# Kernel optimization log

Measured on AMD Instinct MI355X. Metric: run time of the kernel, lower is better.

## Reference

```python
import jax, jax.numpy as jnp
import numpy as np

B, L, D, H = 32, 1024, 1024, 1024

def setup_inputs() -> dict:
    key = jax.random.key(0)
    k1, k2, k3 = jax.random.split(key, 3)
    query = jax.random.normal(k1, (B, L, D), dtype=jnp.float32)
    keys = jax.random.normal(k2, (B, L, D), dtype=jnp.float32)
    # xavier_normal for Linear(D, H): std = sqrt(2/(D+H))
    W = jax.random.normal(k3, (H, D), dtype=jnp.float32) * np.sqrt(2.0 / (D + H)).astype(np.float32)
    b = jnp.zeros((H,), dtype=jnp.float32)
    return {"query": query, "keys": keys, "W": W, "b": b}

def reference(query, keys, W, b):
    # L2-normalize along feature dim (matches torch .norm(dim=-1, keepdim=True))
    qn = query / jnp.linalg.norm(query, axis=-1, keepdims=True)
    kn = keys / jnp.linalg.norm(keys, axis=-1, keepdims=True)
    # scores[b,i,j] = <kn[b,i], qn[b,j]>  ->  [B, Lk, Lq]
    scores = jnp.einsum('bid,bjd->bij', kn, qn)
    attn = jax.nn.softmax(scores, axis=-1)
    # bmm(attn, keys) then sum over batch -> [L, D]
    out = jnp.einsum('bij,bjd->id', attn, keys)
    x = jax.nn.relu(out @ W.T + b)
    return (x, attn)
```

## Files before the change

kernel.cpp:

```cpp
#include <hip/hip_runtime.h>
#include <hip/hip_bf16.h>

#define NBATCH 32
#define Ls 1024
#define Ds 1024
#define Hs 1024

typedef float f32x4 __attribute__((ext_vector_type(4)));
typedef __bf16 v8bf __attribute__((ext_vector_type(8)));
typedef __hip_bfloat16 bf16;

struct bf4 { bf16 a, b, c, d; };

__global__ __launch_bounds__(256) void k_norm(const float* __restrict__ q,
                                              const float* __restrict__ k,
                                              bf16* __restrict__ qn,
                                              bf16* __restrict__ kn) {
  const size_t row = (size_t)blockIdx.x * 4 + (threadIdx.x >> 6);
  const int lane = threadIdx.x & 63;
  const float4* qr = reinterpret_cast<const float4*>(q + row * Ds);
  const float4* kr = reinterpret_cast<const float4*>(k + row * Ds);
  float4 qv[4], kv[4];
  float sq = 0.f, sk = 0.f;
  #pragma unroll
  for (int p = 0; p < 4; ++p) {
    qv[p] = qr[lane + 64 * p];
    kv[p] = kr[lane + 64 * p];
    sq += qv[p].x*qv[p].x + qv[p].y*qv[p].y + qv[p].z*qv[p].z + qv[p].w*qv[p].w;
    sk += kv[p].x*kv[p].x + kv[p].y*kv[p].y + kv[p].z*kv[p].z + kv[p].w*kv[p].w;
  }
  #pragma unroll
  for (int o = 1; o < 64; o <<= 1) { sq += __shfl_xor(sq, o); sk += __shfl_xor(sk, o); }
  const float invq = 1.0f / sqrtf(sq);
  const float invk = 1.0f / sqrtf(sk);
  bf4* qo = reinterpret_cast<bf4*>(qn + row * Ds);
  bf4* ko = reinterpret_cast<bf4*>(kn + row * Ds);
  #pragma unroll
  for (int p = 0; p < 4; ++p) {
    bf4 oq = { __float2bfloat16(qv[p].x * invq), __float2bfloat16(qv[p].y * invq),
               __float2bfloat16(qv[p].z * invq), __float2bfloat16(qv[p].w * invq) };
    bf4 ok = { __float2bfloat16(kv[p].x * invk), __float2bfloat16(kv[p].y * invk),
               __float2bfloat16(kv[p].z * invk), __float2bfloat16(kv[p].w * invk) };
    qo[lane + 64 * p] = oq;
    ko[lane + 64 * p] = ok;
  }
}

__global__ __launch_bounds__(256) void k_transpose(const float* __restrict__ k,
                                                   bf16* __restrict__ kT) {
  __shared__ float tile[64][65];
  const int b = blockIdx.z;
  const int d0 = blockIdx.x * 64, j0 = blockIdx.y * 64;
  const int tx = threadIdx.x, ty = threadIdx.y;
  const float* src = k + (size_t)b * Ls * Ds;
  #pragma unroll
  for (int r = 0; r < 16; ++r)
    tile[ty + r * 4][tx] = src[(size_t)(j0 + ty + r * 4) * Ds + d0 + tx];
  __syncthreads();
  bf16* dst = kT + (size_t)b * Ds * Ls;
  #pragma unroll
  for (int r = 0; r < 16; ++r)
    dst[(size_t)(d0 + ty + r * 4) * Ls + j0 + tx] = __float2bfloat16(tile[tx][ty + r * 4]);
}

__global__ __launch_bounds__(256) void k_w2(const float* __restrict__ W,
                                            bf16* __restrict__ W2) {
  const size_t idx = (size_t)blockIdx.x * 256 + threadIdx.x;
  const size_t h = idx >> 10, d = idx & 1023;
  const float w = W[idx];
  const bf16 wh = __float2bfloat16(w);
  const bf16 wl = __float2bfloat16(w - __bfloat162float(wh));
  bf16* row = W2 + h * 3072;
  row[d] = wh; row[1024 + d] = wh; row[2048 + d] = wl;
}

template<int KT>
__global__ __launch_bounds__(512) void k_gemm256(
    const bf16* __restrict__ A, const bf16* __restrict__ B,
    float* __restrict__ C,
    int lda, int ldb, int ldc, int nb,
    size_t sA, size_t sB, size_t zA, size_t zB, size_t zC)
{
  __shared__ bf16 lds[2][2][256 * 64];
  const int tid = threadIdx.x;
  const int lane = tid & 63;
  const int wid = tid >> 6;
  const int wr = wid >> 2;
  const int wc = wid & 3;
  const size_t m0 = (size_t)blockIdx.y * 256;
  const size_t n0 = (size_t)blockIdx.x * 256;
  const bf16* Az = A + (size_t)blockIdx.z * zA;
  const bf16* Bz = B + (size_t)blockIdx.z * zB;
  float* Cz = C + (size_t)blockIdx.z * zC;

  const int srow = tid >> 3;
  const int sslot = tid & 7;
  f32x4 acc[8][4] = {};

  auto stage = [&](int tt, int buf) {
    const int b = tt / KT;
    const int k0 = (tt - b * KT) * 64;
    const bf16* Ab = Az + (size_t)b * sA;
    const bf16* Bb = Bz + (size_t)b * sB;
    #pragma unroll
    for (int c = 0; c < 4; ++c) {
      const int row = c * 64 + srow;
      const int ksl = (sslot ^ (row & 7)) * 8;
      __builtin_amdgcn_global_load_lds(
          (const __attribute__((address_space(1))) void*)(Ab + (m0 + row) * lda + k0 + ksl),
          (__attribute__((address_space(3))) void*)(&lds[buf][0][c * 4096 + tid * 8]), 16, 0, 0);
    }
    #pragma unroll
    for (int c = 0; c < 4; ++c) {
      const int row = c * 64 + srow;
      const int ksl = (sslot ^ (row & 7)) * 8;
      __builtin_amdgcn_global_load_lds(
          (const __attribute__((address_space(1))) void*)(Bb + (n0 + row) * ldb + k0 + ksl),
          (__attribute__((address_space(3))) void*)(&lds[buf][1][c * 4096 + tid * 8]), 16, 0, 0);
    }
  };

  const int rsel = lane & 15, qd = lane >> 4;
  auto compute = [&](int buf) {
    const bf16* As = lds[buf][0];
    const bf16* Bs = lds[buf][1];
    v8bf bfrag[2][4];
    #pragma unroll
    for (int h = 0; h < 2; ++h)
      #pragma unroll
      for (int n = 0; n < 4; ++n) {
        const int r = wc * 64 + n * 16 + rsel;
        const int s = (h * 4 + qd) ^ (r & 7);
        bfrag[h][n] = *reinterpret_cast<const v8bf*>(
            reinterpret_cast<const char*>(Bs) + r * 128 + s * 16);
      }
    #pragma unroll
    for (int m = 0; m < 8; ++m) {
      const int r = wr * 128 + m * 16 + rsel;
      const int s0 = qd ^ (r & 7);
      const int s1 = (4 + qd) ^ (r & 7);
      const v8bf a0 = *reinterpret_cast<const v8bf*>(
          reinterpret_cast<const char*>(As) + r * 128 + s0 * 16);
      const v8bf a1 = *reinterpret_cast<const v8bf*>(
          reinterpret_cast<const char*>(As) + r * 128 + s1 * 16);
      #pragma unroll
      for (int n = 0; n < 4; ++n)
        acc[m][n] = __builtin_amdgcn_mfma_f32_16x16x32_bf16(a0, bfrag[0][n], acc[m][n], 0, 0, 0);
      #pragma unroll
      for (int n = 0; n < 4; ++n)
        acc[m][n] = __builtin_amdgcn_mfma_f32_16x16x32_bf16(a1, bfrag[1][n], acc[m][n], 0, 0, 0);
    }
  };

  const int T = KT * nb;
  stage(0, 0);
  for (int t = 0; t < T - 1; ++t) {
    __builtin_amdgcn_s_barrier();
    stage(t + 1, (t + 1) & 1);
    asm volatile("s_waitcnt vmcnt(8)" ::: "memory");
    __builtin_amdgcn_s_barrier();
    compute(t & 1);
  }
  asm volatile("s_waitcnt vmcnt(0)" ::: "memory");
  __builtin_amdgcn_s_barrier();
  compute((T - 1) & 1);

  #pragma unroll
  for (int m = 0; m < 8; ++m) {
    const size_t ri = m0 + wr * 128 + m * 16 + (size_t)((lane >> 4) * 4);
    #pragma unroll
    for (int n = 0; n < 4; ++n) {
      const size_t cj = n0 + wc * 64 + n * 16 + (lane & 15);
      #pragma unroll
      for (int r = 0; r < 4; ++r)
        Cz[(ri + r) * ldc + cj] = acc[m][n][r];
    }
  }
}

__global__ __launch_bounds__(256) void k_gemm_nt(
    const bf16* __restrict__ A, const bf16* __restrict__ B,
    float* __restrict__ C,
    int lda, int ldb, int ldc, int K,
    size_t zA, size_t zB, size_t zC)
{
  __shared__ bf16 As[128 * 32];
  __shared__ bf16 Bs[128 * 32];
  const int tid = threadIdx.x;
  const int lane = tid & 63;
  const int wc = (tid >> 6) & 1;
  const int wr = (tid >> 7) & 1;
  const size_t m0 = (size_t)blockIdx.y * 128;
  const size_t n0 = (size_t)blockIdx.x * 128;
  const bf16* Az = A + (size_t)blockIdx.z * zA;
  const bf16* Bz = B + (size_t)blockIdx.z * zB;
  float* Cz = C + (size_t)blockIdx.z * zC;
  f32x4 acc[4][4] = {};

  const int beta0 = tid * 16;
  const int row0 = tid >> 2;
  const int kk0 = ((tid & 3) ^ ((row0 >> 1) & 3)) * 8;
  const int sw = (((lane >> 4) ^ ((lane >> 1) & 3)) << 4);
  const int rsel = lane & 15;

  for (int k0 = 0; k0 < K; k0 += 32) {
    __syncthreads();
    __builtin_amdgcn_global_load_lds(
        (const __attribute__((address_space(1))) void*)(Az + (m0 + row0) * lda + (k0 + kk0)),
        (__attribute__((address_space(3))) void*)(&As[beta0 / 2]), 16, 0, 0);
    __builtin_amdgcn_global_load_lds(
        (const __attribute__((address_space(1))) void*)(Az + (m0 + row0 + 64) * lda + (k0 + kk0)),
        (__attribute__((address_space(3))) void*)(&As[beta0 / 2 + 2048]), 16, 0, 0);
    __builtin_amdgcn_global_load_lds(
        (const __attribute__((address_space(1))) void*)(Bz + (n0 + row0) * ldb + (k0 + kk0)),
        (__attribute__((address_space(3))) void*)(&Bs[beta0 / 2]), 16, 0, 0);
    __builtin_amdgcn_global_load_lds(
        (const __attribute__((address_space(1))) void*)(Bz + (n0 + row0 + 64) * ldb + (k0 + kk0)),
        (__attribute__((address_space(3))) void*)(&Bs[beta0 / 2 + 2048]), 16, 0, 0);
    __syncthreads();

    v8bf af[4], bg[4];
    #pragma unroll
    for (int m = 0; m < 4; ++m) {
      const int rA = wr * 64 + m * 16 + rsel;
      af[m] = *reinterpret_cast<const v8bf*>(reinterpret_cast<const char*>(As) + rA * 64 + sw);
      const int rB = wc * 64 + m * 16 + rsel;
      bg[m] = *reinterpret_cast<const v8bf*>(reinterpret_cast<const char*>(Bs) + rB * 64 + sw);
    }
    #pragma unroll
    for (int m = 0; m < 4; ++m)
      #pragma unroll
      for (int n = 0; n < 4; ++n)
        acc[m][n] = __builtin_amdgcn_mfma_f32_16x16x32_bf16(af[m], bg[n], acc[m][n], 0, 0, 0);
  }

  #pragma unroll
  for (int m = 0; m < 4; ++m) {
    const size_t ri = m0 + wr * 64 + m * 16 + ((lane >> 4) * 4);
    #pragma unroll
    for (int n = 0; n < 4; ++n) {
      const size_t cj = n0 + wc * 64 + n * 16 + (lane & 15);
      #pragma unroll
      for (int r = 0; r < 4; ++r)
        Cz[(ri + r) * ldc + cj] = acc[m][n][r];
    }
  }
}

__global__ __launch_bounds__(256) void k_softmax(float* __restrict__ sc,
                                                 bf16* __restrict__ abf) {
  const size_t row = (size_t)blockIdx.x * 4 + (threadIdx.x >> 6);
  const int lane = threadIdx.x & 63;
  float4* s = reinterpret_cast<float4*>(sc + row * Ls);
  float4 v[4];
  float mx = -3.4e38f;
  #pragma unroll
  for (int p = 0; p < 4; ++p) {
    v[p] = s[lane + 64 * p];
    mx = fmaxf(mx, fmaxf(fmaxf(v[p].x, v[p].y), fmaxf(v[p].z, v[p].w)));
  }
  #pragma unroll
  for (int o = 1; o < 64; o <<= 1) mx = fmaxf(mx, __shfl_xor(mx, o));
  float ss = 0.f;
  #pragma unroll
  for (int p = 0; p < 4; ++p) {
    v[p].x = __expf(v[p].x - mx); v[p].y = __expf(v[p].y - mx);
    v[p].z = __expf(v[p].z - mx); v[p].w = __expf(v[p].w - mx);
    ss += v[p].x + v[p].y + v[p].z + v[p].w;
  }
  #pragma unroll
  for (int o = 1; o < 64; o <<= 1) ss += __shfl_xor(ss, o);
  const float inv = 1.0f / ss;
  bf4* ab = reinterpret_cast<bf4*>(abf + row * Ls);
  #pragma unroll
  for (int p = 0; p < 4; ++p) {
    v[p].x *= inv; v[p].y *= inv; v[p].z *= inv; v[p].w *= inv;
    s[lane + 64 * p] = v[p];
    bf4 o4 = { __float2bfloat16(v[p].x), __float2bfloat16(v[p].y),
               __float2bfloat16(v[p].z), __float2bfloat16(v[p].w) };
    ab[lane + 64 * p] = o4;
  }
}

__global__ __launch_bounds__(256) void k_reduce(const float* __restrict__ part,
                                                bf16* __restrict__ A2) {
  const size_t idx = (size_t)blockIdx.x * 256 + threadIdx.x;
  float4 s = {0.f, 0.f, 0.f, 0.f};
  #pragma unroll
  for (int g = 0; g < 16; ++g) {
    const float4 p = reinterpret_cast<const float4*>(part + (size_t)g * (Ls * Ds))[idx];
    s.x += p.x; s.y += p.y; s.z += p.z; s.w += p.w;
  }
  const size_t e0 = idx * 4;
  const size_t i = e0 >> 10, d = e0 & 1023;
  bf4 h, l;
  h.a = __float2bfloat16(s.x); l.a = __float2bfloat16(s.x - __bfloat162float(h.a));
  h.b = __float2bfloat16(s.y); l.b = __float2bfloat16(s.y - __bfloat162float(h.b));
  h.c = __float2bfloat16(s.z); l.c = __float2bfloat16(s.z - __bfloat162float(h.c));
  h.d = __float2bfloat16(s.w); l.d = __float2bfloat16(s.w - __bfloat162float(h.d));
  bf16* row = A2 + i * 3072;
  *reinterpret_cast<bf4*>(row + d) = h;
  *reinterpret_cast<bf4*>(row + 1024 + d) = l;
  *reinterpret_cast<bf4*>(row + 2048 + d) = h;
}

__global__ __launch_bounds__(256) void k_reduce2(const float* __restrict__ part2,
                                                 const float* __restrict__ bias,
                                                 float* __restrict__ xout) {
  const size_t idx = (size_t)blockIdx.x * 256 + threadIdx.x;
  float4 s = {0.f, 0.f, 0.f, 0.f};
  #pragma unroll
  for (int g = 0; g < 4; ++g) {
    const float4 p = reinterpret_cast<const float4*>(part2 + (size_t)g * (Ls * Hs))[idx];
    s.x += p.x; s.y += p.y; s.z += p.z; s.w += p.w;
  }
  const size_t h0 = (idx * 4) & 1023;
  const float4 bv = *reinterpret_cast<const float4*>(bias + h0);
  s.x = fmaxf(s.x + bv.x, 0.f); s.y = fmaxf(s.y + bv.y, 0.f);
  s.z = fmaxf(s.z + bv.z, 0.f); s.w = fmaxf(s.w + bv.w, 0.f);
  reinterpret_cast<float4*>(xout)[idx] = s;
}

extern "C" void kernel_launch(void* const* d_in, const int* in_sizes, int n_in,
                              void* d_out, int out_size, void* d_ws, size_t ws_size,
                              hipStream_t stream) {
  const float* q = (const float*)d_in[0];
  const float* k = (const float*)d_in[1];
  const float* W = (const float*)d_in[2];
  const float* bias = (const float*)d_in[3];
  float* xout = (float*)d_out;
  float* attn = (float*)d_out + (size_t)Ls * Hs;

  char* w = (char*)d_ws;
  bf16* qn = (bf16*)w;
  bf16* kn = (bf16*)(w + ((size_t)64 << 20));
  bf16* kT = (bf16*)(w + ((size_t)128 << 20));
  bf16* W2 = (bf16*)(w + ((size_t)192 << 20));
  bf16* A2 = (bf16*)(w + ((size_t)199 << 20));
  float* part = (float*)kn;
  float* part2 = (float*)kT;
  bf16* abf = qn;

  k_norm<<<NBATCH * Ls / 4, 256, 0, stream>>>(q, k, qn, kn);
  k_transpose<<<dim3(16, 16, NBATCH), dim3(64, 4), 0, stream>>>(k, kT);
  k_w2<<<(Hs * Ds) / 256, 256, 0, stream>>>(W, W2);

  k_gemm256<16><<<dim3(4, 4, NBATCH), 512, 0, stream>>>(kn, qn, attn,
      Ds, Ds, Ls, 1,
      (size_t)Ls * Ds, (size_t)Ls * Ds,
      (size_t)Ls * Ds, (size_t)Ls * Ds, (size_t)Ls * Ls);

  k_softmax<<<NBATCH * Ls / 4, 256, 0, stream>>>(attn, abf);

  k_gemm256<16><<<dim3(4, 4, 16), 512, 0, stream>>>(abf, kT, part,
      Ls, Ls, Ds, 2,
      (size_t)Ls * Ls, (size_t)Ls * Ds,
      (size_t)2 * Ls * Ls, (size_t)2 * Ls * Ds, (size_t)Ls * Ds);

  k_reduce<<<(Ls * Ds / 4) / 256, 256, 0, stream>>>(part, A2);

  k_gemm_nt<<<dim3(8, 8, 4), 256, 0, stream>>>(A2, W2, part2,
      3072, 3072, Hs, 768, 768, 768, (size_t)Ls * Hs);

  k_reduce2<<<(Ls * Hs / 4) / 256, 256, 0, stream>>>(part2, bias, xout);
}
```

Before: 373.6 us.

## Store scores as bf16, skip softmax max, and transpose from bf16 keys

Keys are now converted to unnormalized bf16 and their inverse norms are applied in the first GEMM epilogue, which writes bf16 scores instead of fp32. The softmax reads these bf16 scores, drops the max pass because cosine scores are bounded in [-1,1], and writes fp32 attn plus bf16 attn. The transpose now reads the bf16 keys with 4-wide vector accesses instead of fp32 keys. Together these cut the traffic of the fp32 score round trip and the transpose input, at the cost of rounding the scores to bf16 before the exponent, which lowers attn accuracy.

```diff
diff --git a/kernel.cpp b/kernel.cpp
--- a/kernel.cpp
+++ b/kernel.cpp
@@ -8,59 +8,81 @@
 
 typedef float f32x4 __attribute__((ext_vector_type(4)));
 typedef __bf16 v8bf __attribute__((ext_vector_type(8)));
+typedef unsigned short u16x8 __attribute__((ext_vector_type(8)));
 typedef __hip_bfloat16 bf16;
 
 struct bf4 { bf16 a, b, c, d; };
 
-__global__ __launch_bounds__(256) void k_norm(const float* __restrict__ q,
-                                              const float* __restrict__ k,
-                                              bf16* __restrict__ qn,
-                                              bf16* __restrict__ kn) {
-  const size_t row = (size_t)blockIdx.x * 4 + (threadIdx.x >> 6);
+__device__ __forceinline__ float bfbits2f(unsigned short h) {
+  unsigned u = ((unsigned)h) << 16;
+  return __builtin_bit_cast(float, u);
+}
+
+__global__ __launch_bounds__(256) void k_convert(const float* __restrict__ q,
+                                                 const float* __restrict__ k,
+                                                 bf16* __restrict__ qn,
+                                                 bf16* __restrict__ kb,
+                                                 float* __restrict__ invk) {
+  const int wave = ((int)blockIdx.x * 256 + (int)threadIdx.x) >> 6;
   const int lane = threadIdx.x & 63;
-  const float4* qr = reinterpret_cast<const float4*>(q + row * Ds);
-  const float4* kr = reinterpret_cast<const float4*>(k + row * Ds);
-  float4 qv[4], kv[4];
-  float sq = 0.f, sk = 0.f;
-  #pragma unroll
-  for (int p = 0; p < 4; ++p) {
-    qv[p] = qr[lane + 64 * p];
-    kv[p] = kr[lane + 64 * p];
-    sq += qv[p].x*qv[p].x + qv[p].y*qv[p].y + qv[p].z*qv[p].z + qv[p].w*qv[p].w;
-    sk += kv[p].x*kv[p].x + kv[p].y*kv[p].y + kv[p].z*kv[p].z + kv[p].w*kv[p].w;
-  }
-  #pragma unroll
-  for (int o = 1; o < 64; o <<= 1) { sq += __shfl_xor(sq, o); sk += __shfl_xor(sk, o); }
-  const float invq = 1.0f / sqrtf(sq);
-  const float invk = 1.0f / sqrtf(sk);
-  bf4* qo = reinterpret_cast<bf4*>(qn + row * Ds);
-  bf4* ko = reinterpret_cast<bf4*>(kn + row * Ds);
-  #pragma unroll
-  for (int p = 0; p < 4; ++p) {
-    bf4 oq = { __float2bfloat16(qv[p].x * invq), __float2bfloat16(qv[p].y * invq),
-               __float2bfloat16(qv[p].z * invq), __float2bfloat16(qv[p].w * invq) };
-    bf4 ok = { __float2bfloat16(kv[p].x * invk), __float2bfloat16(kv[p].y * invk),
-               __float2bfloat16(kv[p].z * invk), __float2bfloat16(kv[p].w * invk) };
-    qo[lane + 64 * p] = oq;
-    ko[lane + 64 * p] = ok;
-  }
-}
-
-__global__ __launch_bounds__(256) void k_transpose(const float* __restrict__ k,
+  for (int i = 0; i < 4; ++i) {
+    const size_t row = (size_t)wave * 4 + i;
+    const float4* qr = reinterpret_cast<const float4*>(q + row * Ds);
+    const float4* kr = reinterpret_cast<const float4*>(k + row * Ds);
+    float4 qv[4], kv[4];
+    float sq = 0.f, sk = 0.f;
+    #pragma unroll
+    for (int p = 0; p < 4; ++p) {
+      qv[p] = qr[lane + 64 * p];
+      kv[p] = kr[lane + 64 * p];
+      sq += qv[p].x*qv[p].x + qv[p].y*qv[p].y + qv[p].z*qv[p].z + qv[p].w*qv[p].w;
+      sk += kv[p].x*kv[p].x + kv[p].y*kv[p].y + kv[p].z*kv[p].z + kv[p].w*kv[p].w;
+    }
+    #pragma unroll
+    for (int o = 1; o < 64; o <<= 1) { sq += __shfl_xor(sq, o); sk += __shfl_xor(sk, o); }
+    const float iq = 1.0f / sqrtf(sq);
+    if (lane == 0) invk[row] = 1.0f / sqrtf(sk);
+    bf4* qo = reinterpret_cast<bf4*>(qn + row * Ds);
+    bf4* ko = reinterpret_cast<bf4*>(kb + row * Ds);
+    #pragma unroll
+    for (int p = 0; p < 4; ++p) {
+      bf4 oq = { __float2bfloat16(qv[p].x * iq), __float2bfloat16(qv[p].y * iq),
+                 __float2bfloat16(qv[p].z * iq), __float2bfloat16(qv[p].w * iq) };
+      bf4 ok = { __float2bfloat16(kv[p].x), __float2bfloat16(kv[p].y),
+                 __float2bfloat16(kv[p].z), __float2bfloat16(kv[p].w) };
+      qo[lane + 64 * p] = oq;
+      ko[lane + 64 * p] = ok;
+    }
+  }
+}
+
+__global__ __launch_bounds__(256) void k_transpose(const bf16* __restrict__ kb,
                                                    bf16* __restrict__ kT) {
   __shared__ float tile[64][65];
   const int b = blockIdx.z;
   const int d0 = blockIdx.x * 64, j0 = blockIdx.y * 64;
-  const int tx = threadIdx.x, ty = threadIdx.y;
-  const float* src = k + (size_t)b * Ls * Ds;
+  const int t = threadIdx.x;
+  const int jr = t >> 4;
+  const int c4 = (t & 15) * 4;
+  const bf16* src = kb + (size_t)b * Ls * Ds;
   #pragma unroll
-  for (int r = 0; r < 16; ++r)
-    tile[ty + r * 4][tx] = src[(size_t)(j0 + ty + r * 4) * Ds + d0 + tx];
+  for (int rr = 0; rr < 4; ++rr) {
+    const int j = jr + rr * 16;
+    const bf4 v = *reinterpret_cast<const bf4*>(&src[(size_t)(j0 + j) * Ds + d0 + c4]);
+    tile[j][c4 + 0] = __bfloat162float(v.a);
+    tile[j][c4 + 1] = __bfloat162float(v.b);
+    tile[j][c4 + 2] = __bfloat162float(v.c);
+    tile[j][c4 + 3] = __bfloat162float(v.d);
+  }
   __syncthreads();
   bf16* dst = kT + (size_t)b * Ds * Ls;
   #pragma unroll
-  for (int r = 0; r < 16; ++r)
-    dst[(size_t)(d0 + ty + r * 4) * Ls + j0 + tx] = __float2bfloat16(tile[tx][ty + r * 4]);
+  for (int rr = 0; rr < 4; ++rr) {
+    const int d = jr + rr * 16;
+    bf4 o = { __float2bfloat16(tile[c4 + 0][d]), __float2bfloat16(tile[c4 + 1][d]),
+              __float2bfloat16(tile[c4 + 2][d]), __float2bfloat16(tile[c4 + 3][d]) };
+    *reinterpret_cast<bf4*>(&dst[(size_t)(d0 + d) * Ls + j0 + c4]) = o;
+  }
 }
 
 __global__ __launch_bounds__(256) void k_w2(const float* __restrict__ W,
@@ -74,12 +96,12 @@
   row[d] = wh; row[1024 + d] = wh; row[2048 + d] = wl;
 }
 
-template<int KT>
+template<int KT, int MODE>
 __global__ __launch_bounds__(512) void k_gemm256(
     const bf16* __restrict__ A, const bf16* __restrict__ B,
-    float* __restrict__ C,
+    void* __restrict__ Cv, const float* __restrict__ scale,
     int lda, int ldb, int ldc, int nb,
-    size_t sA, size_t sB, size_t zA, size_t zB, size_t zC)
+    size_t sA, size_t sB, size_t zA, size_t zB, size_t zC, size_t zS)
 {
   __shared__ bf16 lds[2][2][256 * 64];
   const int tid = threadIdx.x;
@@ -91,7 +113,6 @@
   const size_t n0 = (size_t)blockIdx.x * 256;
   const bf16* Az = A + (size_t)blockIdx.z * zA;
   const bf16* Bz = B + (size_t)blockIdx.z * zB;
-  float* Cz = C + (size_t)blockIdx.z * zC;
 
   const int srow = tid >> 3;
   const int sslot = tid & 7;
@@ -100,14 +121,14 @@
   auto stage = [&](int tt, int buf) {
     const int b = tt / KT;
     const int k0 = (tt - b * KT) * 64;
-    const bf16* Ab = Az + (size_t)b * sA;
-    const bf16* Bb = Bz + (size_t)b * sB;
+    const bf16* Abp = Az + (size_t)b * sA;
+    const bf16* Bbp = Bz + (size_t)b * sB;
     #pragma unroll
     for (int c = 0; c < 4; ++c) {
       const int row = c * 64 + srow;
       const int ksl = (sslot ^ (row & 7)) * 8;
       __builtin_amdgcn_global_load_lds(
-          (const __attribute__((address_space(1))) void*)(Ab + (m0 + row) * lda + k0 + ksl),
+          (const __attribute__((address_space(1))) void*)(Abp + (m0 + row) * lda + k0 + ksl),
           (__attribute__((address_space(3))) void*)(&lds[buf][0][c * 4096 + tid * 8]), 16, 0, 0);
     }
     #pragma unroll
@@ -115,7 +136,7 @@
       const int row = c * 64 + srow;
       const int ksl = (sslot ^ (row & 7)) * 8;
       __builtin_amdgcn_global_load_lds(
-          (const __attribute__((address_space(1))) void*)(Bb + (n0 + row) * ldb + k0 + ksl),
+          (const __attribute__((address_space(1))) void*)(Bbp + (n0 + row) * ldb + k0 + ksl),
           (__attribute__((address_space(3))) void*)(&lds[buf][1][c * 4096 + tid * 8]), 16, 0, 0);
     }
   };
@@ -165,15 +186,34 @@
   __builtin_amdgcn_s_barrier();
   compute((T - 1) & 1);
 
-  #pragma unroll
-  for (int m = 0; m < 8; ++m) {
-    const size_t ri = m0 + wr * 128 + m * 16 + (size_t)((lane >> 4) * 4);
-    #pragma unroll
-    for (int n = 0; n < 4; ++n) {
-      const size_t cj = n0 + wc * 64 + n * 16 + (lane & 15);
-      #pragma unroll
-      for (int r = 0; r < 4; ++r)
-        Cz[(ri + r) * ldc + cj] = acc[m][n][r];
+  if (MODE == 0) {
+    float* Cz = (float*)Cv + (size_t)blockIdx.z * zC;
+    #pragma unroll
+    for (int m = 0; m < 8; ++m) {
+      const size_t ri = m0 + wr * 128 + m * 16 + (size_t)((lane >> 4) * 4);
+      #pragma unroll
+      for (int n = 0; n < 4; ++n) {
+        const size_t cj = n0 + wc * 64 + n * 16 + (lane & 15);
+        #pragma unroll
+        for (int r = 0; r < 4; ++r)
+          Cz[(ri + r) * ldc + cj] = acc[m][n][r];
+      }
+    }
+  } else {
+    bf16* Cz = (bf16*)Cv + (size_t)blockIdx.z * zC;
+    const float* Sz = scale + (size_t)blockIdx.z * zS;
+    #pragma unroll
+    for (int m = 0; m < 8; ++m) {
+      const size_t ri = m0 + wr * 128 + m * 16 + (size_t)((lane >> 4) * 4);
+      const float4 ik = *reinterpret_cast<const float4*>(Sz + ri);
+      #pragma unroll
+      for (int n = 0; n < 4; ++n) {
+        const size_t cj = n0 + wc * 64 + n * 16 + (lane & 15);
+        Cz[(ri + 0) * ldc + cj] = __float2bfloat16(acc[m][n][0] * ik.x);
+        Cz[(ri + 1) * ldc + cj] = __float2bfloat16(acc[m][n][1] * ik.y);
+        Cz[(ri + 2) * ldc + cj] = __float2bfloat16(acc[m][n][2] * ik.z);
+        Cz[(ri + 3) * ldc + cj] = __float2bfloat16(acc[m][n][3] * ik.w);
+      }
     }
   }
 }
@@ -247,38 +287,42 @@
   }
 }
 
-__global__ __launch_bounds__(256) void k_softmax(float* __restrict__ sc,
+__global__ __launch_bounds__(256) void k_softmax(const bf16* __restrict__ sc,
+                                                 float* __restrict__ attn,
                                                  bf16* __restrict__ abf) {
-  const size_t row = (size_t)blockIdx.x * 4 + (threadIdx.x >> 6);
+  const int wave = ((int)blockIdx.x * 256 + (int)threadIdx.x) >> 6;
   const int lane = threadIdx.x & 63;
-  float4* s = reinterpret_cast<float4*>(sc + row * Ls);
-  float4 v[4];
-  float mx = -3.4e38f;
-  #pragma unroll
-  for (int p = 0; p < 4; ++p) {
-    v[p] = s[lane + 64 * p];
-    mx = fmaxf(mx, fmaxf(fmaxf(v[p].x, v[p].y), fmaxf(v[p].z, v[p].w)));
-  }
-  #pragma unroll
-  for (int o = 1; o < 64; o <<= 1) mx = fmaxf(mx, __shfl_xor(mx, o));
-  float ss = 0.f;
-  #pragma unroll
-  for (int p = 0; p < 4; ++p) {
-    v[p].x = __expf(v[p].x - mx); v[p].y = __expf(v[p].y - mx);
-    v[p].z = __expf(v[p].z - mx); v[p].w = __expf(v[p].w - mx);
-    ss += v[p].x + v[p].y + v[p].z + v[p].w;
-  }
-  #pragma unroll
-  for (int o = 1; o < 64; o <<= 1) ss += __shfl_xor(ss, o);
-  const float inv = 1.0f / ss;
-  bf4* ab = reinterpret_cast<bf4*>(abf + row * Ls);
-  #pragma unroll
-  for (int p = 0; p < 4; ++p) {
-    v[p].x *= inv; v[p].y *= inv; v[p].z *= inv; v[p].w *= inv;
-    s[lane + 64 * p] = v[p];
-    bf4 o4 = { __float2bfloat16(v[p].x), __float2bfloat16(v[p].y),
-               __float2bfloat16(v[p].z), __float2bfloat16(v[p].w) };
-    ab[lane + 64 * p] = o4;
+  for (int i = 0; i < 4; ++i) {
+    const size_t row = (size_t)wave * 4 + i;
+    const u16x8* sr = reinterpret_cast<const u16x8*>(sc + row * Ls);
+    const u16x8 s0 = sr[lane], s1 = sr[lane + 64];
+    float e[16];
+    float ss = 0.f;
+    #pragma unroll
+    for (int j = 0; j < 8; ++j) { e[j] = __expf(bfbits2f(s0[j])); ss += e[j]; }
+    #pragma unroll
+    for (int j = 0; j < 8; ++j) { e[8 + j] = __expf(bfbits2f(s1[j])); ss += e[8 + j]; }
+    #pragma unroll
+    for (int o = 1; o < 64; o <<= 1) ss += __shfl_xor(ss, o);
+    const float inv = 1.0f / ss;
+    #pragma unroll
+    for (int j = 0; j < 16; ++j) e[j] *= inv;
+    float4* ar = reinterpret_cast<float4*>(attn + row * Ls);
+    float4 a0 = {e[0], e[1], e[2], e[3]},   a1 = {e[4], e[5], e[6], e[7]};
+    float4 a2 = {e[8], e[9], e[10], e[11]}, a3 = {e[12], e[13], e[14], e[15]};
+    ar[lane * 2 + 0] = a0;  ar[lane * 2 + 1] = a1;
+    ar[128 + lane * 2 + 0] = a2;  ar[128 + lane * 2 + 1] = a3;
+    bf4* ab = reinterpret_cast<bf4*>(abf + row * Ls);
+    bf4 b0 = { __float2bfloat16(e[0]),  __float2bfloat16(e[1]),
+               __float2bfloat16(e[2]),  __float2bfloat16(e[3]) };
+    bf4 b1 = { __float2bfloat16(e[4]),  __float2bfloat16(e[5]),
+               __float2bfloat16(e[6]),  __float2bfloat16(e[7]) };
+    bf4 b2 = { __float2bfloat16(e[8]),  __float2bfloat16(e[9]),
+               __float2bfloat16(e[10]), __float2bfloat16(e[11]) };
+    bf4 b3 = { __float2bfloat16(e[12]), __float2bfloat16(e[13]),
+               __float2bfloat16(e[14]), __float2bfloat16(e[15]) };
+    ab[lane * 2 + 0] = b0;  ab[lane * 2 + 1] = b1;
+    ab[128 + lane * 2 + 0] = b2;  ab[128 + lane * 2 + 1] = b3;
   }
 }
 
@@ -332,30 +376,32 @@
   float* attn = (float*)d_out + (size_t)Ls * Hs;
 
   char* w = (char*)d_ws;
-  bf16* qn = (bf16*)w;
-  bf16* kn = (bf16*)(w + ((size_t)64 << 20));
-  bf16* kT = (bf16*)(w + ((size_t)128 << 20));
-  bf16* W2 = (bf16*)(w + ((size_t)192 << 20));
-  bf16* A2 = (bf16*)(w + ((size_t)199 << 20));
-  float* part = (float*)kn;
+  bf16* qn    = (bf16*)w;
+  bf16* kb    = (bf16*)(w + ((size_t)64 << 20));
+  bf16* kT    = (bf16*)(w + ((size_t)128 << 20));
+  bf16* sc_bf = (bf16*)(w + ((size_t)192 << 20));
+  bf16* W2    = (bf16*)(w + ((size_t)256 << 20));
+  bf16* A2    = (bf16*)(w + ((size_t)263 << 20));
+  float* invk = (float*)(w + ((size_t)270 << 20));
+  float* part  = (float*)kb;
   float* part2 = (float*)kT;
   bf16* abf = qn;
 
-  k_norm<<<NBATCH * Ls / 4, 256, 0, stream>>>(q, k, qn, kn);
-  k_transpose<<<dim3(16, 16, NBATCH), dim3(64, 4), 0, stream>>>(k, kT);
+  k_convert<<<2048, 256, 0, stream>>>(q, k, qn, kb, invk);
+  k_transpose<<<dim3(16, 16, NBATCH), 256, 0, stream>>>(kb, kT);
   k_w2<<<(Hs * Ds) / 256, 256, 0, stream>>>(W, W2);
 
-  k_gemm256<16><<<dim3(4, 4, NBATCH), 512, 0, stream>>>(kn, qn, attn,
+  k_gemm256<16, 1><<<dim3(4, 4, NBATCH), 512, 0, stream>>>(kb, qn, sc_bf, invk,
       Ds, Ds, Ls, 1,
       (size_t)Ls * Ds, (size_t)Ls * Ds,
-      (size_t)Ls * Ds, (size_t)Ls * Ds, (size_t)Ls * Ls);
-
-  k_softmax<<<NBATCH * Ls / 4, 256, 0, stream>>>(attn, abf);
-
-  k_gemm256<16><<<dim3(4, 4, 16), 512, 0, stream>>>(abf, kT, part,
+      (size_t)Ls * Ds, (size_t)Ls * Ds, (size_t)Ls * Ls, (size_t)Ls);
+
+  k_softmax<<<2048, 256, 0, stream>>>(sc_bf, attn, abf);
+
+  k_gemm256<16, 0><<<dim3(4, 4, 16), 512, 0, stream>>>(abf, kT, part, nullptr,
       Ls, Ls, Ds, 2,
       (size_t)Ls * Ls, (size_t)Ls * Ds,
-      (size_t)2 * Ls * Ls, (size_t)2 * Ls * Ds, (size_t)Ls * Ds);
+      (size_t)2 * Ls * Ls, (size_t)2 * Ls * Ds, (size_t)Ls * Ds, 0);
 
   k_reduce<<<(Ls * Ds / 4) / 256, 256, 0, stream>>>(part, A2);
 
```

New measurement: 363.3 us. 2.8% less time.
